# Kernel tuning notes

Measured on AMD Instinct MI355X. Metric: run time of the kernel, lower is better.

The kernel has to match this reference:

```python
import jax, jax.numpy as jnp
import numpy as np

B = 128          # graphs
N = 512          # nodes per graph
NT = B * N       # total nodes = 65536
E = NT * 16      # total edges = 1048576
IN = 64
H = 128
OUT = 2
L = 4            # num_layers
RATIO = 0.8


def setup_inputs() -> dict:
    key = jax.random.key(0)
    ks = jax.random.split(key, 20)

    def w(k, shape, fan_in):
        return jax.random.normal(k, shape, jnp.float32) / np.sqrt(fan_in)

    x = jax.random.normal(ks[0], (NT, IN), jnp.float32)
    edge_index = jax.random.randint(ks[1], (2, E), 0, NT, dtype=jnp.int32)
    batch = (jnp.arange(NT) // N).astype(jnp.int32)  # equal-size graphs

    return {
        "x": x,
        "edge_index": edge_index,
        "batch": batch,
        # conv1: GraphConv(IN, H, aggr='mean') -> lin_rel (w/ bias) + lin_root (no bias)
        "W1_rel": w(ks[2], (IN, H), IN),
        "W1_root": w(ks[3], (IN, H), IN),
        "b1": jnp.zeros((H,), jnp.float32),
        # convs[0..2]: GraphConv(H, H, aggr='mean'), stacked
        "Wc_rel": w(ks[4], (L - 1, H, H), H),
        "Wc_root": w(ks[5], (L - 1, H, H), H),
        "bc": jnp.zeros((L - 1, H), jnp.float32),
        # SAGPooling score GNN: GraphConv(H, 1) with default aggr='add'
        "pw_rel": w(ks[6], (H,), H),
        "pw_root": w(ks[7], (H,), H),
        "pb": jnp.zeros((1,), jnp.float32),
        # MLP head
        "lin1_W": w(ks[8], (L * H, H), L * H),
        "lin1_b": jnp.zeros((H,), jnp.float32),
        "lin2_W": w(ks[9], (H, OUT), H),
        "lin2_b": jnp.zeros((OUT,), jnp.float32),
    }


def _graph_conv_mean(x, src, dst, emask, W_rel, W_root, b, n):
    # PyG GraphConv: lin_rel(mean_{j->i} x_j) + lin_root(x_i); masked edges excluded.
    msg = x[src] * emask[:, None]                                  # [E, D] gather
    s = jax.ops.segment_sum(msg, dst, num_segments=n)              # [n, D] scatter-add
    cnt = jax.ops.segment_sum(emask, dst, num_segments=n)          # [n]
    agg = s / jnp.maximum(cnt, 1.0)[:, None]                       # zero for isolated nodes
    return agg @ W_rel + x @ W_root + b


def reference(x, edge_index, batch, W1_rel, W1_root, b1, Wc_rel, Wc_root, bc,
              pw_rel, pw_root, pb, lin1_W, lin1_b, lin2_W, lin2_b):
    src = edge_index[0]
    dst = edge_index[1]
    emask = jnp.ones((E,), jnp.float32)
    n = NT
    npg = N  # nodes per graph (all graphs equal size)

    h = jax.nn.relu(_graph_conv_mean(x, src, dst, emask, W1_rel, W1_root, b1, n))
    xs = [h.reshape(B, npg, H).mean(axis=1)]  # global_mean_pool

    for i in range(L - 1):
        h = jax.nn.relu(_graph_conv_mean(h, src, dst, emask, Wc_rel[i], Wc_root[i], bc[i], n))
        xs.append(h.reshape(B, npg, H).mean(axis=1))
        if i % 2 == 0 and i < L - 2:
            # ---- SAGPooling: score via GraphConv(H,1) with add aggregation ----
            smsg = jax.ops.segment_sum(h[src] * emask[:, None], dst, num_segments=n)
            score = smsg @ pw_rel + h @ pw_root + pb[0]            # [n]
            k = int(np.ceil(RATIO * npg))
            topv, topi = jax.lax.top_k(score.reshape(B, npg), k)   # per-graph top-k
            perm = (jnp.arange(B)[:, None] * npg + topi).reshape(-1)  # global kept ids
            h = h[perm] * jnp.tanh(topv.reshape(-1))[:, None]
            # remap edges; edges touching dropped nodes get masked out
            node_map = jnp.full((n,), -1, jnp.int32).at[perm].set(
                jnp.arange(B * k, dtype=jnp.int32))
            ns, nd = node_map[src], node_map[dst]
            keep = ((ns >= 0) & (nd >= 0)).astype(jnp.float32)
            emask = emask * keep
            src = jnp.where(ns >= 0, ns, 0)
            dst = jnp.where(nd >= 0, nd, 0)
            n = B * k
            npg = k

    xcat = jnp.concatenate(xs, axis=-1)                            # JumpingKnowledge 'cat'
    out = jax.nn.relu(xcat @ lin1_W + lin1_b)
    # dropout is identity in eval mode
    out = out @ lin2_W + lin2_b
    return jax.nn.log_softmax(out, axis=-1)
```

## Files before the change

kernel.cpp:

```cpp
#include <hip/hip_runtime.h>
#include <math.h>

#define NT 65536
#define EE 1048576
#define NB 128
#define KK 410
#define HH 128

typedef short bf16x8 __attribute__((ext_vector_type(8)));
typedef float f32x4 __attribute__((ext_vector_type(4)));

__device__ unsigned short g_xb[(size_t)NT * 64];
__device__ unsigned short g_hb1[(size_t)NT * HH];
__device__ unsigned short g_hb2[(size_t)NT * HH];
__device__ unsigned short g_wt1[128 * 128];
__device__ unsigned short g_wtc[3 * 128 * 256];
__device__ unsigned short g_csr1u[EE];
__device__ unsigned short g_keptu[NT];
__device__ unsigned int g_ebuck[EE];
__device__ int g_bcnt[128];
__device__ int g_bbase[129];
__device__ int g_bcur[128];
__device__ float g_trel[NT];
__device__ float g_troot[NT];
__device__ float g_gatef[NT];
__device__ float g_kinv[NT];
__device__ float g_xc4[4 * NB * 4 * 128];
__device__ int g_rows1[NT + 1];

__device__ __forceinline__ unsigned short* ubuf(int id) {
    switch (id) {
        case 0: return g_xb;
        case 1: return g_hb1;
        case 2: return g_hb2;
        case 3: return g_wt1;
        case 4: return g_wtc;
    }
    return g_xb;
}

__device__ __forceinline__ float b2f(unsigned short u) {
    union { unsigned int i; float f; } v;
    v.i = ((unsigned int)u) << 16;
    return v.f;
}
__device__ __forceinline__ unsigned short f2b(float f) {
    unsigned int x = __float_as_uint(f);
    unsigned int r = x + 0x7fffu + ((x >> 16) & 1u);
    return (unsigned short)(r >> 16);
}
__device__ __forceinline__ bf16x8 scale8(bf16x8 a, float g) {
    bf16x8 r;
#pragma unroll
    for (int i = 0; i < 8; i++) {
        unsigned short u = (unsigned short)a[i];
        r[i] = (short)f2b(b2f(u) * g);
    }
    return r;
}

__global__ void k_prep(const float* __restrict__ x,
                       const float* __restrict__ W1r, const float* __restrict__ W1o,
                       const float* __restrict__ Wcr, const float* __restrict__ Wco) {
    int tid = blockIdx.x * 256 + threadIdx.x;
    if (tid < 1048576) {
        float4 v = *(const float4*)&x[(size_t)tid * 4];
        unsigned int lo = (unsigned int)f2b(v.x) | ((unsigned int)f2b(v.y) << 16);
        unsigned int hi = (unsigned int)f2b(v.z) | ((unsigned int)f2b(v.w) << 16);
        *(uint2*)&g_xb[(size_t)tid * 4] = make_uint2(lo, hi);
    } else if (tid < 1048576 + 16384) {
        int r = tid - 1048576;
        int k = r & 127, n = r >> 7;
        float v = (k < 64) ? W1r[k * 128 + n] : W1o[(k - 64) * 128 + n];
        g_wt1[n * 128 + k] = f2b(v);
    } else if (tid < 1048576 + 16384 + 98304) {
        int r = tid - (1048576 + 16384);
        int l = r >> 15;
        int k = r & 255, n = (r >> 8) & 127;
        float v = (k < 128) ? Wcr[l * 16384 + k * 128 + n]
                            : Wco[l * 16384 + (k - 128) * 128 + n];
        g_wtc[l * 32768 + n * 256 + k] = f2b(v);
    } else if (tid < 1048576 + 16384 + 98304 + 128) {
        g_bcnt[tid - (1048576 + 16384 + 98304)] = 0;
    }
}

__global__ __launch_bounds__(256) void k_bhist(const int* __restrict__ dst) {
    __shared__ int h[128];
    if (threadIdx.x < 128) h[threadIdx.x] = 0;
    __syncthreads();
    int e0 = (blockIdx.x * 256 + threadIdx.x) * 4;
    int4 d = *(const int4*)&dst[e0];
    atomicAdd(&h[d.x >> 9], 1);
    atomicAdd(&h[d.y >> 9], 1);
    atomicAdd(&h[d.z >> 9], 1);
    atomicAdd(&h[d.w >> 9], 1);
    __syncthreads();
    if (threadIdx.x < 128 && h[threadIdx.x]) atomicAdd(&g_bcnt[threadIdx.x], h[threadIdx.x]);
}

__global__ __launch_bounds__(128) void k_bscan() {
    __shared__ int s[128];
    int t = threadIdx.x;
    int v = g_bcnt[t];
    s[t] = v;
    __syncthreads();
    for (int off = 1; off < 128; off <<= 1) {
        int u = (t >= off) ? s[t - off] : 0;
        __syncthreads();
        s[t] += u;
        __syncthreads();
    }
    g_bbase[t] = s[t] - v;
    g_bcur[t] = s[t] - v;
    if (t == 127) g_bbase[128] = s[127];
}

__global__ __launch_bounds__(256) void k_bscatter(const int* __restrict__ src,
                                                  const int* __restrict__ dst) {
    __shared__ int h[128];
    __shared__ int base[128];
    if (threadIdx.x < 128) h[threadIdx.x] = 0;
    __syncthreads();
    int e0 = (blockIdx.x * 256 + threadIdx.x) * 4;
    int4 s = *(const int4*)&src[e0];
    int4 d = *(const int4*)&dst[e0];
    int b0 = d.x >> 9, b1 = d.y >> 9, b2 = d.z >> 9, b3 = d.w >> 9;
    atomicAdd(&h[b0], 1);
    atomicAdd(&h[b1], 1);
    atomicAdd(&h[b2], 1);
    atomicAdd(&h[b3], 1);
    __syncthreads();
    if (threadIdx.x < 128) {
        int c = h[threadIdx.x];
        base[threadIdx.x] = c ? atomicAdd(&g_bcur[threadIdx.x], c) : 0;
        h[threadIdx.x] = 0;
    }
    __syncthreads();
    int r0 = atomicAdd(&h[b0], 1);
    g_ebuck[base[b0] + r0] = ((unsigned int)(d.x & 511) << 16) | (unsigned int)s.x;
    int r1 = atomicAdd(&h[b1], 1);
    g_ebuck[base[b1] + r1] = ((unsigned int)(d.y & 511) << 16) | (unsigned int)s.y;
    int r2 = atomicAdd(&h[b2], 1);
    g_ebuck[base[b2] + r2] = ((unsigned int)(d.z & 511) << 16) | (unsigned int)s.z;
    int r3 = atomicAdd(&h[b3], 1);
    g_ebuck[base[b3] + r3] = ((unsigned int)(d.w & 511) << 16) | (unsigned int)s.w;
}

__global__ __launch_bounds__(512) void k_bcsr() {
    __shared__ int hist[512];
    __shared__ int offs[512];
    __shared__ int cur[512];
    int g = blockIdx.x, t = threadIdx.x;
    hist[t] = 0;
    cur[t] = 0;
    __syncthreads();
    int b0 = g_bbase[g], b1 = g_bbase[g + 1];
    for (int e = b0 + t; e < b1; e += 512) {
        unsigned int p = g_ebuck[e];
        atomicAdd(&hist[p >> 16], 1);
    }
    __syncthreads();
    int v = hist[t];
    offs[t] = v;
    __syncthreads();
    for (int off = 1; off < 512; off <<= 1) {
        int u = (t >= off) ? offs[t - off] : 0;
        __syncthreads();
        offs[t] += u;
        __syncthreads();
    }
    int excl = offs[t] - v;
    g_rows1[g * 512 + t] = b0 + excl;
    if (t == 511) g_rows1[g * 512 + 512] = b0 + excl + v;
    __syncthreads();
    offs[t] = excl;
    __syncthreads();
    for (int e = b0 + t; e < b1; e += 512) {
        unsigned int p = g_ebuck[e];
        int dl = p >> 16;
        int r = atomicAdd(&cur[dl], 1);
        g_csr1u[b0 + offs[dl] + r] = (unsigned short)(p & 0xFFFFu);
    }
}

template <int KA, int KB, int KC, int GATED, int MASKED, int DOTS, int BGATE>
__global__ __launch_bounds__(256) void k_conv(int hId, int bId, int wId, int wOfs,
                                              const float* __restrict__ bias, int outId,
                                              int sec,
                                              const float* __restrict__ pwr,
                                              const float* __restrict__ pwt) {
    constexpr int STR = KA + 8;
    __shared__ unsigned short lds_a[128 * STR];
    __shared__ float s[128];
    const unsigned short* h = ubuf(hId);
    const unsigned short* Bp = ubuf(bId);
    const unsigned short* Wt = ubuf(wId) + wOfs;
    unsigned short* out = ubuf(outId);
    int rowbase = blockIdx.x * 128;

    {
        constexpr int TPN = KA / 8;
        constexpr int RPP = 256 / TPN;
        int local = threadIdx.x / TPN;
        int t = threadIdx.x % TPN;
        const unsigned short* ht = h + t * 8;
#pragma unroll 1
        for (int pass = 0; pass < 128 / RPP; pass++) {
            int rl = pass * RPP + local;
            int node = rowbase + rl;
            int r0 = g_rows1[node], r1 = g_rows1[node + 1];
            float kinv_pre = (KC == 2) ? g_kinv[node] : 0.f;
            float acc[8];
#pragma unroll
            for (int i = 0; i < 8; i++) acc[i] = 0.f;
            int kc = 0;
#define ACCV(v, gf)                                              \
    acc[0] += gf * b2f((unsigned short)(v.x & 0xffff));          \
    acc[1] += gf * b2f((unsigned short)(v.x >> 16));             \
    acc[2] += gf * b2f((unsigned short)(v.y & 0xffff));          \
    acc[3] += gf * b2f((unsigned short)(v.y >> 16));             \
    acc[4] += gf * b2f((unsigned short)(v.z & 0xffff));          \
    acc[5] += gf * b2f((unsigned short)(v.z >> 16));             \
    acc[6] += gf * b2f((unsigned short)(v.w & 0xffff));          \
    acc[7] += gf * b2f((unsigned short)(v.w >> 16));
            int e = r0;
            for (; e + 4 <= r1; e += 4) {
                int i0 = g_csr1u[e], i1 = g_csr1u[e + 1];
                int i2 = g_csr1u[e + 2], i3 = g_csr1u[e + 3];
                uint4 v0 = *(const uint4*)&ht[(size_t)i0 * KA];
                uint4 v1 = *(const uint4*)&ht[(size_t)i1 * KA];
                uint4 v2 = *(const uint4*)&ht[(size_t)i2 * KA];
                uint4 v3 = *(const uint4*)&ht[(size_t)i3 * KA];
                float g0 = GATED ? g_gatef[i0] : 1.0f;
                float g1 = GATED ? g_gatef[i1] : 1.0f;
                float g2 = GATED ? g_gatef[i2] : 1.0f;
                float g3 = GATED ? g_gatef[i3] : 1.0f;
                if (KC == 1)
                    kc += (int)g_keptu[i0] + (int)g_keptu[i1]
                        + (int)g_keptu[i2] + (int)g_keptu[i3];
                ACCV(v0, g0) ACCV(v1, g1) ACCV(v2, g2) ACCV(v3, g3)
            }
            for (; e < r1; e++) {
                int i0 = g_csr1u[e];
                uint4 v0 = *(const uint4*)&ht[(size_t)i0 * KA];
                float g0 = GATED ? g_gatef[i0] : 1.0f;
                if (KC == 1) kc += (int)g_keptu[i0];
                ACCV(v0, g0)
            }
#undef ACCV
            float inv;
            if (KC == 0) {
                int c = r1 - r0;
                inv = 1.0f / (float)(c > 0 ? c : 1);
            } else if (KC == 1) {
                inv = 1.0f / (float)(kc > 0 ? kc : 1);
                if (t == 0) g_kinv[node] = inv;
            } else {
                inv = kinv_pre;
            }
            uint4 o;
            o.x = (unsigned int)f2b(acc[0] * inv) | ((unsigned int)f2b(acc[1] * inv) << 16);
            o.y = (unsigned int)f2b(acc[2] * inv) | ((unsigned int)f2b(acc[3] * inv) << 16);
            o.z = (unsigned int)f2b(acc[4] * inv) | ((unsigned int)f2b(acc[5] * inv) << 16);
            o.w = (unsigned int)f2b(acc[6] * inv) | ((unsigned int)f2b(acc[7] * inv) << 16);
            *(uint4*)&lds_a[rl * STR + t * 8] = o;
        }
    }
    __syncthreads();

    const int K = KA + KB;
    int lane = threadIdx.x & 63;
    int w = threadIdx.x >> 6;
    int n16 = lane & 15, quad = lane >> 4;
    int rowloc = w * 32;
    int rowg = rowbase + rowloc;
    int g = blockIdx.x >> 2, qb = blockIdx.x & 3;
    float ga0 = BGATE ? g_gatef[rowg + n16] : 1.0f;
    float ga1 = BGATE ? g_gatef[rowg + 16 + n16] : 1.0f;
    f32x4 acc[2][8];
#pragma unroll
    for (int rt = 0; rt < 2; rt++)
#pragma unroll
        for (int ct = 0; ct < 8; ct++)
#pragma unroll
            for (int i = 0; i < 4; i++) acc[rt][ct][i] = 0.f;

#pragma unroll
    for (int ks = 0; ks < K / 32; ks++) {
        int k0 = ks * 32;
        bf16x8 a0, a1;
        if (k0 < KA) {
            a0 = *(const bf16x8*)&lds_a[(rowloc + n16) * STR + k0 + quad * 8];
            a1 = *(const bf16x8*)&lds_a[(rowloc + 16 + n16) * STR + k0 + quad * 8];
        } else {
            int kk = k0 - KA;
            a0 = *(const bf16x8*)&Bp[(size_t)(rowg + n16) * KB + kk + quad * 8];
            a1 = *(const bf16x8*)&Bp[(size_t)(rowg + 16 + n16) * KB + kk + quad * 8];
            if (BGATE) { a0 = scale8(a0, ga0); a1 = scale8(a1, ga1); }
        }
#pragma unroll
        for (int ct = 0; ct < 8; ct++) {
            bf16x8 b = *(const bf16x8*)&Wt[(size_t)(ct * 16 + n16) * K + k0 + quad * 8];
            acc[0][ct] = __builtin_amdgcn_mfma_f32_16x16x32_bf16(a0, b, acc[0][ct], 0, 0, 0);
            acc[1][ct] = __builtin_amdgcn_mfma_f32_16x16x32_bf16(a1, b, acc[1][ct], 0, 0, 0);
        }
    }

    if (threadIdx.x < 128) s[threadIdx.x] = 0.f;
#pragma unroll
    for (int rt = 0; rt < 2; rt++) {
        float m[4];
#pragma unroll
        for (int i = 0; i < 4; i++) {
            int r = rowg + rt * 16 + quad * 4 + i;
            m[i] = (!MASKED || g_keptu[r]) ? 1.0f : 0.0f;
        }
#pragma unroll
        for (int ct = 0; ct < 8; ct++) {
            int c = ct * 16 + n16;
            float bv = bias[c];
#pragma unroll
            for (int i = 0; i < 4; i++) {
                int r = rowg + rt * 16 + quad * 4 + i;
                float v = fmaxf(acc[rt][ct][i] + bv, 0.f) * m[i];
                acc[rt][ct][i] = v;
                out[(size_t)r * 128 + c] = f2b(v);
            }
        }
    }
    __syncthreads();

#pragma unroll
    for (int ct = 0; ct < 8; ct++) {
        float p = 0.f;
#pragma unroll
        for (int rt = 0; rt < 2; rt++)
#pragma unroll
            for (int i = 0; i < 4; i++) p += acc[rt][ct][i];
        p += __shfl_xor(p, 16);
        p += __shfl_xor(p, 32);
        if (quad == 0) atomicAdd(&s[ct * 16 + n16], p);
    }

    if (DOTS) {
        float pr[8], pt[8];
#pragma unroll
        for (int ct = 0; ct < 8; ct++) {
            pr[ct] = pwr[ct * 16 + n16];
            pt[ct] = pwt[ct * 16 + n16];
        }
#pragma unroll
        for (int rt = 0; rt < 2; rt++)
#pragma unroll
            for (int i = 0; i < 4; i++) {
                float dr = 0.f, dt = 0.f;
#pragma unroll
                for (int ct = 0; ct < 8; ct++) {
                    dr += acc[rt][ct][i] * pr[ct];
                    dt += acc[rt][ct][i] * pt[ct];
                }
                dr += __shfl_xor(dr, 1); dt += __shfl_xor(dt, 1);
                dr += __shfl_xor(dr, 2); dt += __shfl_xor(dt, 2);
                dr += __shfl_xor(dr, 4); dt += __shfl_xor(dt, 4);
                dr += __shfl_xor(dr, 8); dt += __shfl_xor(dt, 8);
                if (n16 == 0) {
                    int r = rowg + rt * 16 + quad * 4 + i;
                    g_trel[r] = dr;
                    g_troot[r] = dt;
                }
            }
    }
    __syncthreads();
    if (threadIdx.x < 128)
        g_xc4[((sec * NB + g) * 4 + qb) * 128 + threadIdx.x] = s[threadIdx.x];
}

__global__ __launch_bounds__(256) void k_topk(const float* __restrict__ pb) {
    __shared__ float sv[512];
    __shared__ int si[512];
    int g = blockIdx.x, t = threadIdx.x;
    float pbv = pb[0];
    for (int l = t; l < 512; l += 256) {
        int node = g * 512 + l;
        int r0 = g_rows1[node], r1 = g_rows1[node + 1];
        float s = 0.f;
        int e = r0;
        for (; e + 4 <= r1; e += 4) {
            float s0 = g_trel[g_csr1u[e]];
            float s1 = g_trel[g_csr1u[e + 1]];
            float s2 = g_trel[g_csr1u[e + 2]];
            float s3 = g_trel[g_csr1u[e + 3]];
            s += (s0 + s1) + (s2 + s3);
        }
        for (; e < r1; e++) s += g_trel[g_csr1u[e]];
        sv[l] = s + g_troot[node] + pbv;
        si[l] = l;
    }
    __syncthreads();
    for (int k = 2; k <= 512; k <<= 1) {
        for (int j = k >> 1; j > 0; j >>= 1) {
            for (int i = t; i < 512; i += 256) {
                int p = i ^ j;
                if (p > i) {
                    float va = sv[i], vb = sv[p];
                    int ia = si[i], ib = si[p];
                    bool aFirst = (va > vb) || (va == vb && ia < ib);
                    bool up = ((i & k) == 0);
                    if (up != aFirst) { sv[i] = vb; sv[p] = va; si[i] = ib; si[p] = ia; }
                }
            }
            __syncthreads();
        }
    }
    for (int r = t; r < 512; r += 256) {
        int old = g * 512 + si[r];
        if (r < KK) {
            g_gatef[old] = tanhf(sv[r]);
            g_keptu[old] = 1;
        } else {
            g_gatef[old] = 0.f;
            g_keptu[old] = 0;
        }
    }
}

__global__ __launch_bounds__(128) void k_head(const float* __restrict__ W1, const float* __restrict__ b1,
                                              const float* __restrict__ W2, const float* __restrict__ b2,
                                              float* __restrict__ out) {
    __shared__ float xr[512];
    __shared__ float r0[128], r1[128];
    int g = blockIdx.x, t = threadIdx.x;
    for (int i = t; i < 512; i += 128) {
        int sec = i >> 7, c = i & 127;
        const float* p = &g_xc4[((sec * NB + g) * 4) * 128 + c];
        float v = p[0] + p[128] + p[256] + p[384];
        float inv = (sec < 2) ? (1.0f / 512.0f) : (1.0f / 410.0f);
        xr[i] = v * inv;
    }
    __syncthreads();
    float acc = b1[t];
    for (int k = 0; k < 512; k++) acc += xr[k] * W1[k * 128 + t];
    acc = fmaxf(acc, 0.f);
    r0[t] = acc * W2[t * 2 + 0];
    r1[t] = acc * W2[t * 2 + 1];
    __syncthreads();
    for (int off = 64; off > 0; off >>= 1) {
        if (t < off) { r0[t] += r0[t + off]; r1[t] += r1[t + off]; }
        __syncthreads();
    }
    if (t == 0) {
        float z0 = r0[0] + b2[0], z1 = r1[0] + b2[1];
        float m = fmaxf(z0, z1);
        float l = m + logf(expf(z0 - m) + expf(z1 - m));
        out[g * 2 + 0] = z0 - l;
        out[g * 2 + 1] = z1 - l;
    }
}

extern "C" void kernel_launch(void* const* d_in, const int* in_sizes, int n_in,
                              void* d_out, int out_size, void* d_ws, size_t ws_size,
                              hipStream_t stream) {
    const float* x = (const float*)d_in[0];
    const int* ei = (const int*)d_in[1];
    const int* src = ei;
    const int* dst = ei + EE;
    const float* W1r = (const float*)d_in[3];
    const float* W1o = (const float*)d_in[4];
    const float* b1 = (const float*)d_in[5];
    const float* Wcr = (const float*)d_in[6];
    const float* Wco = (const float*)d_in[7];
    const float* bc = (const float*)d_in[8];
    const float* pwr = (const float*)d_in[9];
    const float* pwt = (const float*)d_in[10];
    const float* pb = (const float*)d_in[11];
    const float* l1W = (const float*)d_in[12];
    const float* l1b = (const float*)d_in[13];
    const float* l2W = (const float*)d_in[14];
    const float* l2b = (const float*)d_in[15];
    float* out = (float*)d_out;

    k_prep<<<(1048576 + 16384 + 98304 + 128 + 255) / 256, 256, 0, stream>>>(x, W1r, W1o, Wcr, Wco);

    k_bhist<<<1024, 256, 0, stream>>>(dst);
    k_bscan<<<1, 128, 0, stream>>>();
    k_bscatter<<<1024, 256, 0, stream>>>(src, dst);
    k_bcsr<<<128, 512, 0, stream>>>();

    k_conv<64, 64, 0, 0, 0, 0, 0><<<512, 256, 0, stream>>>(0, 0, 3, 0, b1, 1, 0, pwr, pwt);

    k_conv<128, 128, 0, 0, 0, 1, 0><<<512, 256, 0, stream>>>(1, 1, 4, 0, bc, 2, 1, pwr, pwt);

    k_topk<<<NB, 256, 0, stream>>>(pb);

    k_conv<128, 128, 1, 1, 1, 0, 1><<<512, 256, 0, stream>>>(2, 2, 4, 32768, bc + 128, 1, 2, pwr, pwt);

    k_conv<128, 128, 2, 0, 1, 0, 0><<<512, 256, 0, stream>>>(1, 1, 4, 65536, bc + 256, 2, 3, pwr, pwt);

    k_head<<<NB, 128, 0, stream>>>(l1W, l1b, l2W, l2b, out);
}
```

Baseline: 495.1 us.

## Split neighbor aggregation from GEMM using feature-sliced node layouts

Neighbor mean aggregation moves out of the fused conv kernel into a separate k_agg kernel. It works on feature-sliced copies of node features (8 slices of 8 or 16 features per node), so each gather pass touches a compact slice that can stay resident in L2. The aggregated result goes to a slice-major global buffer, which the new k_mm MFMA kernel reads directly instead of staging through LDS. Kept-neighbor counts and gating get their own small kernels. The cost is extra kernel launches, extra global writes and reads for the intermediate buffers, and a scattered sliced-copy store in the GEMM epilogue.

```diff
diff --git a/kernel.cpp b/kernel.cpp
--- a/kernel.cpp
+++ b/kernel.cpp
@@ -9,12 +9,16 @@
 
 typedef short bf16x8 __attribute__((ext_vector_type(8)));
 typedef float f32x4 __attribute__((ext_vector_type(4)));
-
-__device__ unsigned short g_xb[(size_t)NT * 64];
-__device__ unsigned short g_hb1[(size_t)NT * HH];
-__device__ unsigned short g_hb2[(size_t)NT * HH];
-__device__ unsigned short g_wt1[128 * 128];
-__device__ unsigned short g_wtc[3 * 128 * 256];
+typedef unsigned int u32x4 __attribute__((ext_vector_type(4)));
+
+__device__ __align__(16) unsigned short g_xb[(size_t)NT * 64];
+__device__ __align__(16) unsigned short g_hb1[(size_t)NT * HH];
+__device__ __align__(16) unsigned short g_hb2[(size_t)NT * HH];
+__device__ __align__(16) unsigned short g_wt1[128 * 128];
+__device__ __align__(16) unsigned short g_wtc[3 * 128 * 256];
+__device__ __align__(16) unsigned short g_xbs[(size_t)8 * NT * 8];
+__device__ __align__(16) unsigned short g_hbs[(size_t)8 * NT * 16];
+__device__ __align__(16) unsigned short g_agg[(size_t)16 * NT * 8];
 __device__ unsigned short g_csr1u[EE];
 __device__ unsigned short g_keptu[NT];
 __device__ unsigned int g_ebuck[EE];
@@ -49,6 +53,14 @@
     unsigned int r = x + 0x7fffu + ((x >> 16) & 1u);
     return (unsigned short)(r >> 16);
 }
+__device__ __forceinline__ unsigned int pk2(float a, float b) {
+    return (unsigned int)f2b(a) | ((unsigned int)f2b(b) << 16);
+}
+__device__ __forceinline__ unsigned int mul2(unsigned int wd, float g) {
+    float lo = b2f((unsigned short)(wd & 0xffffu)) * g;
+    float hi = b2f((unsigned short)(wd >> 16)) * g;
+    return pk2(lo, hi);
+}
 __device__ __forceinline__ bf16x8 scale8(bf16x8 a, float g) {
     bf16x8 r;
 #pragma unroll
@@ -65,9 +77,13 @@
     int tid = blockIdx.x * 256 + threadIdx.x;
     if (tid < 1048576) {
         float4 v = *(const float4*)&x[(size_t)tid * 4];
-        unsigned int lo = (unsigned int)f2b(v.x) | ((unsigned int)f2b(v.y) << 16);
-        unsigned int hi = (unsigned int)f2b(v.z) | ((unsigned int)f2b(v.w) << 16);
+        unsigned int lo = pk2(v.x, v.y);
+        unsigned int hi = pk2(v.z, v.w);
         *(uint2*)&g_xb[(size_t)tid * 4] = make_uint2(lo, hi);
+        int node = tid >> 4;
+        int sl = (tid & 15) >> 1;
+        int of = (tid & 1) * 4;
+        *(uint2*)&g_xbs[(((size_t)sl) * NT + node) * 8 + of] = make_uint2(lo, hi);
     } else if (tid < 1048576 + 16384) {
         int r = tid - 1048576;
         int k = r & 127, n = r >> 7;
@@ -184,91 +200,102 @@
     }
 }
 
-template <int KA, int KB, int KC, int GATED, int MASKED, int DOTS, int BGATE>
-__global__ __launch_bounds__(256) void k_conv(int hId, int bId, int wId, int wOfs,
-                                              const float* __restrict__ bias, int outId,
-                                              int sec,
-                                              const float* __restrict__ pwr,
-                                              const float* __restrict__ pwt) {
-    constexpr int STR = KA + 8;
-    __shared__ unsigned short lds_a[128 * STR];
+#define ACCP(wd, J) { acc[J] += b2f((unsigned short)((wd) & 0xffffu)); acc[(J) + 1] += b2f((unsigned short)((wd) >> 16)); }
+#define ACCQ(q, B) ACCP(q.x, B) ACCP(q.y, (B) + 2) ACCP(q.z, (B) + 4) ACCP(q.w, (B) + 6)
+
+template <int F, int DEN>
+__global__ __launch_bounds__(256) void k_agg(int srcId) {
+    const unsigned short* src = (srcId == 0) ? g_xbs : g_hbs;
+    int s = blockIdx.x & 7;
+    int node = (blockIdx.x >> 3) * 256 + threadIdx.x;
+    const unsigned short* sp = src + (size_t)s * NT * F;
+    int r0 = g_rows1[node], r1 = g_rows1[node + 1];
+    float inv;
+    if (DEN) {
+        inv = g_kinv[node];
+    } else {
+        int c = r1 - r0;
+        inv = 1.0f / (float)(c > 0 ? c : 1);
+    }
+    float acc[F];
+#pragma unroll
+    for (int i = 0; i < F; i++) acc[i] = 0.f;
+    int e = r0;
+    for (; e + 2 <= r1; e += 2) {
+        int i0 = g_csr1u[e], i1 = g_csr1u[e + 1];
+        if constexpr (F == 16) {
+            uint4 a0 = *(const uint4*)&sp[(size_t)i0 * 16];
+            uint4 a1 = *(const uint4*)&sp[(size_t)i0 * 16 + 8];
+            uint4 b0 = *(const uint4*)&sp[(size_t)i1 * 16];
+            uint4 b1 = *(const uint4*)&sp[(size_t)i1 * 16 + 8];
+            ACCQ(a0, 0) ACCQ(a1, 8) ACCQ(b0, 0) ACCQ(b1, 8)
+        } else {
+            uint4 a0 = *(const uint4*)&sp[(size_t)i0 * 8];
+            uint4 b0 = *(const uint4*)&sp[(size_t)i1 * 8];
+            ACCQ(a0, 0) ACCQ(b0, 0)
+        }
+    }
+    for (; e < r1; e++) {
+        int i0 = g_csr1u[e];
+        if constexpr (F == 16) {
+            uint4 a0 = *(const uint4*)&sp[(size_t)i0 * 16];
+            uint4 a1 = *(const uint4*)&sp[(size_t)i0 * 16 + 8];
+            ACCQ(a0, 0) ACCQ(a1, 8)
+        } else {
+            uint4 a0 = *(const uint4*)&sp[(size_t)i0 * 8];
+            ACCQ(a0, 0)
+        }
+    }
+    int gb = (F == 16) ? (2 * s) : s;
+    u32x4 o;
+    o[0] = pk2(acc[0] * inv, acc[1] * inv);
+    o[1] = pk2(acc[2] * inv, acc[3] * inv);
+    o[2] = pk2(acc[4] * inv, acc[5] * inv);
+    o[3] = pk2(acc[6] * inv, acc[7] * inv);
+    __builtin_nontemporal_store(o, (u32x4*)&g_agg[((size_t)gb * NT + node) * 8]);
+    if constexpr (F == 16) {
+        u32x4 o2;
+        o2[0] = pk2(acc[8] * inv, acc[9] * inv);
+        o2[1] = pk2(acc[10] * inv, acc[11] * inv);
+        o2[2] = pk2(acc[12] * inv, acc[13] * inv);
+        o2[3] = pk2(acc[14] * inv, acc[15] * inv);
+        __builtin_nontemporal_store(o2, (u32x4*)&g_agg[((size_t)(2 * s + 1) * NT + node) * 8]);
+    }
+}
+
+__global__ __launch_bounds__(256) void k_kinv() {
+    int node = blockIdx.x * 256 + threadIdx.x;
+    int r0 = g_rows1[node], r1 = g_rows1[node + 1];
+    int kc = 0;
+    for (int e = r0; e < r1; e++) kc += (int)g_keptu[g_csr1u[e]];
+    g_kinv[node] = 1.0f / (float)(kc > 0 ? kc : 1);
+}
+
+__global__ __launch_bounds__(256) void k_gateS() {
+    int tid = blockIdx.x * 256 + threadIdx.x;
+    int n = tid >> 3, s = tid & 7;
+    float g = g_gatef[n];
+    const unsigned short* srcp = &g_hb2[(size_t)n * 128 + s * 16];
+    uint4 a = *(const uint4*)srcp;
+    uint4 b = *(const uint4*)(srcp + 8);
+    uint4 oa, ob;
+    oa.x = mul2(a.x, g); oa.y = mul2(a.y, g); oa.z = mul2(a.z, g); oa.w = mul2(a.w, g);
+    ob.x = mul2(b.x, g); ob.y = mul2(b.y, g); ob.z = mul2(b.z, g); ob.w = mul2(b.w, g);
+    unsigned short* d = &g_hbs[((size_t)s * NT + n) * 16];
+    *(uint4*)d = oa;
+    *(uint4*)(d + 8) = ob;
+}
+
+template <int KA, int KB, int MASKED, int DOTS, int BGATE, int WSL>
+__global__ __launch_bounds__(256) void k_mm(int bId, int wId, int wOfs,
+                                            const float* __restrict__ bias, int outId, int sec,
+                                            const float* __restrict__ pwr,
+                                            const float* __restrict__ pwt) {
     __shared__ float s[128];
-    const unsigned short* h = ubuf(hId);
     const unsigned short* Bp = ubuf(bId);
     const unsigned short* Wt = ubuf(wId) + wOfs;
     unsigned short* out = ubuf(outId);
     int rowbase = blockIdx.x * 128;
-
-    {
-        constexpr int TPN = KA / 8;
-        constexpr int RPP = 256 / TPN;
-        int local = threadIdx.x / TPN;
-        int t = threadIdx.x % TPN;
-        const unsigned short* ht = h + t * 8;
-#pragma unroll 1
-        for (int pass = 0; pass < 128 / RPP; pass++) {
-            int rl = pass * RPP + local;
-            int node = rowbase + rl;
-            int r0 = g_rows1[node], r1 = g_rows1[node + 1];
-            float kinv_pre = (KC == 2) ? g_kinv[node] : 0.f;
-            float acc[8];
-#pragma unroll
-            for (int i = 0; i < 8; i++) acc[i] = 0.f;
-            int kc = 0;
-#define ACCV(v, gf)                                              \
-    acc[0] += gf * b2f((unsigned short)(v.x & 0xffff));          \
-    acc[1] += gf * b2f((unsigned short)(v.x >> 16));             \
-    acc[2] += gf * b2f((unsigned short)(v.y & 0xffff));          \
-    acc[3] += gf * b2f((unsigned short)(v.y >> 16));             \
-    acc[4] += gf * b2f((unsigned short)(v.z & 0xffff));          \
-    acc[5] += gf * b2f((unsigned short)(v.z >> 16));             \
-    acc[6] += gf * b2f((unsigned short)(v.w & 0xffff));          \
-    acc[7] += gf * b2f((unsigned short)(v.w >> 16));
-            int e = r0;
-            for (; e + 4 <= r1; e += 4) {
-                int i0 = g_csr1u[e], i1 = g_csr1u[e + 1];
-                int i2 = g_csr1u[e + 2], i3 = g_csr1u[e + 3];
-                uint4 v0 = *(const uint4*)&ht[(size_t)i0 * KA];
-                uint4 v1 = *(const uint4*)&ht[(size_t)i1 * KA];
-                uint4 v2 = *(const uint4*)&ht[(size_t)i2 * KA];
-                uint4 v3 = *(const uint4*)&ht[(size_t)i3 * KA];
-                float g0 = GATED ? g_gatef[i0] : 1.0f;
-                float g1 = GATED ? g_gatef[i1] : 1.0f;
-                float g2 = GATED ? g_gatef[i2] : 1.0f;
-                float g3 = GATED ? g_gatef[i3] : 1.0f;
-                if (KC == 1)
-                    kc += (int)g_keptu[i0] + (int)g_keptu[i1]
-                        + (int)g_keptu[i2] + (int)g_keptu[i3];
-                ACCV(v0, g0) ACCV(v1, g1) ACCV(v2, g2) ACCV(v3, g3)
-            }
-            for (; e < r1; e++) {
-                int i0 = g_csr1u[e];
-                uint4 v0 = *(const uint4*)&ht[(size_t)i0 * KA];
-                float g0 = GATED ? g_gatef[i0] : 1.0f;
-                if (KC == 1) kc += (int)g_keptu[i0];
-                ACCV(v0, g0)
-            }
-#undef ACCV
-            float inv;
-            if (KC == 0) {
-                int c = r1 - r0;
-                inv = 1.0f / (float)(c > 0 ? c : 1);
-            } else if (KC == 1) {
-                inv = 1.0f / (float)(kc > 0 ? kc : 1);
-                if (t == 0) g_kinv[node] = inv;
-            } else {
-                inv = kinv_pre;
-            }
-            uint4 o;
-            o.x = (unsigned int)f2b(acc[0] * inv) | ((unsigned int)f2b(acc[1] * inv) << 16);
-            o.y = (unsigned int)f2b(acc[2] * inv) | ((unsigned int)f2b(acc[3] * inv) << 16);
-            o.z = (unsigned int)f2b(acc[4] * inv) | ((unsigned int)f2b(acc[5] * inv) << 16);
-            o.w = (unsigned int)f2b(acc[6] * inv) | ((unsigned int)f2b(acc[7] * inv) << 16);
-            *(uint4*)&lds_a[rl * STR + t * 8] = o;
-        }
-    }
-    __syncthreads();
-
     const int K = KA + KB;
     int lane = threadIdx.x & 63;
     int w = threadIdx.x >> 6;
@@ -291,8 +318,9 @@
         int k0 = ks * 32;
         bf16x8 a0, a1;
         if (k0 < KA) {
-            a0 = *(const bf16x8*)&lds_a[(rowloc + n16) * STR + k0 + quad * 8];
-            a1 = *(const bf16x8*)&lds_a[(rowloc + 16 + n16) * STR + k0 + quad * 8];
+            int fg = (k0 + quad * 8) >> 3;
+            a0 = *(const bf16x8*)&g_agg[((size_t)fg * NT + rowg + n16) * 8];
+            a1 = *(const bf16x8*)&g_agg[((size_t)fg * NT + rowg + 16 + n16) * 8];
         } else {
             int kk = k0 - KA;
             a0 = *(const bf16x8*)&Bp[(size_t)(rowg + n16) * KB + kk + quad * 8];
@@ -325,7 +353,9 @@
                 int r = rowg + rt * 16 + quad * 4 + i;
                 float v = fmaxf(acc[rt][ct][i] + bv, 0.f) * m[i];
                 acc[rt][ct][i] = v;
-                out[(size_t)r * 128 + c] = f2b(v);
+                unsigned short hv = f2b(v);
+                out[(size_t)r * 128 + c] = hv;
+                if (WSL) g_hbs[((size_t)(c >> 4) * NT + r) * 16 + (c & 15)] = hv;
             }
         }
     }
@@ -487,15 +517,21 @@
     k_bscatter<<<1024, 256, 0, stream>>>(src, dst);
     k_bcsr<<<128, 512, 0, stream>>>();
 
-    k_conv<64, 64, 0, 0, 0, 0, 0><<<512, 256, 0, stream>>>(0, 0, 3, 0, b1, 1, 0, pwr, pwt);
-
-    k_conv<128, 128, 0, 0, 0, 1, 0><<<512, 256, 0, stream>>>(1, 1, 4, 0, bc, 2, 1, pwr, pwt);
+    k_agg<8, 0><<<2048, 256, 0, stream>>>(0);
+    k_mm<64, 64, 0, 0, 0, 1><<<512, 256, 0, stream>>>(0, 3, 0, b1, 1, 0, pwr, pwt);
+
+    k_agg<16, 0><<<2048, 256, 0, stream>>>(1);
+    k_mm<128, 128, 0, 1, 0, 0><<<512, 256, 0, stream>>>(1, 4, 0, bc, 2, 1, pwr, pwt);
 
     k_topk<<<NB, 256, 0, stream>>>(pb);
-
-    k_conv<128, 128, 1, 1, 1, 0, 1><<<512, 256, 0, stream>>>(2, 2, 4, 32768, bc + 128, 1, 2, pwr, pwt);
-
-    k_conv<128, 128, 2, 0, 1, 0, 0><<<512, 256, 0, stream>>>(1, 1, 4, 65536, bc + 256, 2, 3, pwr, pwt);
+    k_kinv<<<NT / 256, 256, 0, stream>>>();
+    k_gateS<<<2048, 256, 0, stream>>>();
+
+    k_agg<16, 1><<<2048, 256, 0, stream>>>(1);
+    k_mm<128, 128, 1, 0, 1, 1><<<512, 256, 0, stream>>>(2, 4, 32768, bc + 128, 1, 2, pwr, pwt);
+
+    k_agg<16, 1><<<2048, 256, 0, stream>>>(1);
+    k_mm<128, 128, 1, 0, 0, 0><<<512, 256, 0, stream>>>(1, 4, 65536, bc + 256, 2, 3, pwr, pwt);
 
     k_head<<<NB, 128, 0, stream>>>(l1W, l1b, l2W, l2b, out);
 }
```

After: 529.3 us. +6.9%, slower.
